# Kernel tuning notes

Measured on AMD Instinct MI355X. Metric: run time of the kernel, lower is better.

Reference implementation:

```python
import jax, jax.numpy as jnp
import numpy as np


def _banded_diag_mean(a, b, r):
    """For each (batch i, row j) return mean of (a[i] @ b[i].T)[j, j-r:j+r+1],
    computed without materializing the LxL matrix. Windows are clipped to
    [max(0,j-r), min(L, j+r+1)].  a, b: [B, L, D]."""
    B, L, _ = a.shape
    sums = jnp.zeros((B, L), a.dtype)
    counts = jnp.zeros((L,), a.dtype)
    for d in range(-r, r + 1):  # small fixed set of 2r+1 diagonals
        if d >= 0:
            dots = jnp.einsum('bld,bld->bl', a[:, :L - d], b[:, d:])
            sums = sums.at[:, :L - d].add(dots)
            counts = counts.at[:L - d].add(1.0)
        else:
            dots = jnp.einsum('bld,bld->bl', a[:, -d:], b[:, :L + d])
            sums = sums.at[:, -d:].add(dots)
            counts = counts.at[-d:].add(1.0)
    return sums / counts


def setup_inputs() -> dict:
    key = jax.random.key(0)
    k1, k2, k3 = jax.random.split(key, 3)
    B, L, D_in, D_feat = 8, 1024, 512, 256
    return {
        'feature1': jax.random.normal(k1, (B, L, D_in), jnp.float32),
        'feature2': jax.random.normal(k2, (B, L, D_in), jnp.float32),
        'W': jax.random.normal(k3, (D_in, D_feat), jnp.float32) / np.sqrt(D_in),
        'b': jnp.zeros((D_feat,), jnp.float32),
        'positive_range_self': 4,
        'positive_range_tgt': 4,
    }


def reference(feature1, feature2, W, b, positive_range_self, positive_range_tgt):
    # MLPLayer projection (shared eval_func for both inputs): linear + relu
    emb_1 = jax.nn.relu(feature1 @ W + b)  # [B, L, Df]
    emb_2 = jax.nn.relu(feature2 @ W + b)  # [B, L, Df]
    B, L, Df = emb_1.shape
    N = B * L

    positive = jnp.einsum('bld,bld->bl', emb_1, emb_2)  # [B, L]
    if positive_range_self > 0:
        positive = positive + _banded_diag_mean(emb_1, emb_1, positive_range_self)
        positive = positive + _banded_diag_mean(emb_2, emb_2, positive_range_self)
    if positive_range_tgt > 0:
        positive = positive + _banded_diag_mean(emb_1, emb_2, positive_range_tgt)
    positive = positive.reshape(N)

    e1 = emb_1.reshape(N, Df)
    e2 = emb_2.reshape(N, Df)
    sim_matrix = e1 @ e2.T  # [N, N]
    negative = jax.nn.logsumexp(sim_matrix, axis=-1) - jnp.log(jnp.asarray(N, sim_matrix.dtype))

    nce_loss = jnp.mean(-positive + negative)
    return nce_loss
```

## Files before the change

kernel.cpp:

```cpp
#include <hip/hip_runtime.h>
#include <hip/hip_bf16.h>
#include <math.h>

#define DIN 512
#define DF 256
#define LSEQ 1024
#define NTOT 8192

typedef __attribute__((ext_vector_type(8))) short short8;
typedef __attribute__((ext_vector_type(4))) short short4v;
typedef __attribute__((ext_vector_type(4))) float f32x4;

__device__ __forceinline__ short f2bf(float x) {
  union { float f; unsigned u; } un; un.f = x;
  unsigned r = un.u + 0x7fffu + ((un.u >> 16) & 1u);
  return (short)(r >> 16);
}
__device__ __forceinline__ float bf2f(short s) {
  union { unsigned u; float f; } un; un.u = ((unsigned)(unsigned short)s) << 16;
  return un.f;
}

typedef __attribute__((address_space(1))) const unsigned char AS1c;
typedef __attribute__((address_space(3))) unsigned char AS3;
__device__ __forceinline__ void gload16(const void* g, void* l) {
  __builtin_amdgcn_global_load_lds((AS1c*)g, (AS3*)l, 16, 0, 0);
}

__global__ __launch_bounds__(256) void prep_w_kernel(const float* __restrict__ W,
                                                     short* __restrict__ Wt) {
  int idx = blockIdx.x * 256 + threadIdx.x;
  int c = idx >> 9;
  int k = idx & (DIN - 1);
  Wt[idx] = f2bf(W[(size_t)k * DF + c]);
}

#define PBM 64
#define PBK 32
#define PPAD 40

__global__ __launch_bounds__(256) void proj_kernel(const float* __restrict__ f1,
                                                   const float* __restrict__ f2,
                                                   const short* __restrict__ Wt,
                                                   const float* __restrict__ bias,
                                                   short* __restrict__ emb1,
                                                   short* __restrict__ emb2) {
  const float* feat = blockIdx.y ? f2 : f1;
  short* emb = blockIdx.y ? emb2 : emb1;
  __shared__ short ldsA[PBM * PPAD];
  __shared__ short ldsB[DF * PPAD];
  const int tid = threadIdx.x;
  const int lane = tid & 63, wv = tid >> 6;
  const int wrow = (wv & 1) * 32, wcol = (wv >> 1) * 128;
  const int l15 = lane & 15, lk = (lane >> 4) * 8;
  const int rowbase = blockIdx.x * PBM;

  f32x4 acc[2][8];
#pragma unroll
  for (int mi = 0; mi < 2; ++mi)
#pragma unroll
    for (int nf = 0; nf < 8; ++nf) acc[mi][nf] = f32x4{0.f, 0.f, 0.f, 0.f};

  for (int kb = 0; kb < DIN; kb += PBK) {
    __syncthreads();
#pragma unroll
    for (int i = 0; i < 2; ++i) {
      int flat = tid * 2 + i;
      int r = flat >> 3, kq = (flat & 7) * 4;
      f32x4 v = *(const f32x4*)(feat + (size_t)(rowbase + r) * DIN + kb + kq);
      short4v h;
      h[0] = f2bf(v[0]); h[1] = f2bf(v[1]); h[2] = f2bf(v[2]); h[3] = f2bf(v[3]);
      *(short4v*)(ldsA + r * PPAD + kq) = h;
    }
#pragma unroll
    for (int i = 0; i < 4; ++i) {
      int flat = tid * 4 + i;
      int c = flat >> 2, kq = (flat & 3) * 8;
      short8 v = *(const short8*)(Wt + (size_t)c * DIN + kb + kq);
      *(short8*)(ldsB + c * PPAD + kq) = v;
    }
    __syncthreads();
    short8 af[2], bf[8];
#pragma unroll
    for (int mi = 0; mi < 2; ++mi)
      af[mi] = *(const short8*)(ldsA + (wrow + mi * 16 + l15) * PPAD + lk);
#pragma unroll
    for (int nf = 0; nf < 8; ++nf)
      bf[nf] = *(const short8*)(ldsB + (wcol + nf * 16 + l15) * PPAD + lk);
#pragma unroll
    for (int mi = 0; mi < 2; ++mi)
#pragma unroll
      for (int nf = 0; nf < 8; ++nf)
        acc[mi][nf] = __builtin_amdgcn_mfma_f32_16x16x32_bf16(af[mi], bf[nf], acc[mi][nf], 0, 0, 0);
  }
  const int r4 = (lane >> 4) * 4;
#pragma unroll
  for (int mi = 0; mi < 2; ++mi) {
    int row0 = rowbase + wrow + mi * 16 + r4;
#pragma unroll
    for (int nf = 0; nf < 8; ++nf) {
      int col = wcol + nf * 16 + l15;
      float bb = bias[col];
#pragma unroll
      for (int r = 0; r < 4; ++r) {
        float v = acc[mi][nf][r] + bb;
        v = v > 0.f ? v : 0.f;
        emb[(size_t)(row0 + r) * DF + col] = f2bf(v);
      }
    }
  }
}

__global__ __launch_bounds__(64) void positive_kernel(const short* __restrict__ emb1,
                                                      const short* __restrict__ emb2,
                                                      const int* __restrict__ prs,
                                                      const int* __restrict__ prt,
                                                      float* __restrict__ pos) {
  const int row = blockIdx.x;
  const int b = row >> 10, j = row & (LSEQ - 1);
  const int lane = threadIdx.x;
  const int rs = prs[0], rt = prt[0];
  float a1[4], a2[4];
  {
    short4v v1 = *(const short4v*)(emb1 + (size_t)row * DF + lane * 4);
    short4v v2 = *(const short4v*)(emb2 + (size_t)row * DF + lane * 4);
#pragma unroll
    for (int i = 0; i < 4; ++i) { a1[i] = bf2f(v1[i]); a2[i] = bf2f(v2[i]); }
  }
  float dot12 = 0.f, p11 = 0.f, p22 = 0.f, p12 = 0.f;
#pragma unroll
  for (int i = 0; i < 4; ++i) dot12 += a1[i] * a2[i];
  int rmax = rs > rt ? rs : rt;
  for (int d = -rmax; d <= rmax; ++d) {
    int k = j + d;
    if (k < 0 || k >= LSEQ) continue;
    size_t koff = (size_t)(b * LSEQ + k) * DF + lane * 4;
    short4v w1 = *(const short4v*)(emb1 + koff);
    short4v w2 = *(const short4v*)(emb2 + koff);
    float d11 = 0.f, d22 = 0.f, d12 = 0.f;
#pragma unroll
    for (int i = 0; i < 4; ++i) {
      float e1k = bf2f(w1[i]), e2k = bf2f(w2[i]);
      d11 += a1[i] * e1k;
      d22 += a2[i] * e2k;
      d12 += a1[i] * e2k;
    }
    if (d >= -rs && d <= rs) { p11 += d11; p22 += d22; }
    if (d >= -rt && d <= rt) { p12 += d12; }
  }
#pragma unroll
  for (int m = 1; m < 64; m <<= 1) {
    dot12 += __shfl_xor(dot12, m);
    p11 += __shfl_xor(p11, m);
    p22 += __shfl_xor(p22, m);
    p12 += __shfl_xor(p12, m);
  }
  if (lane == 0) {
    float res = dot12;
    if (rs > 0) {
      int lo = j - rs < 0 ? 0 : j - rs;
      int hi = j + rs > LSEQ - 1 ? LSEQ - 1 : j + rs;
      res += (p11 + p22) / (float)(hi - lo + 1);
    }
    if (rt > 0) {
      int lo = j - rt < 0 ? 0 : j - rt;
      int hi = j + rt > LSEQ - 1 ? LSEQ - 1 : j + rt;
      res += p12 / (float)(hi - lo + 1);
    }
    pos[row] = res;
  }
}

#define NBM 256
#define NBN 64
#define NCHUNK 16
#define CHW (NTOT / NCHUNK)
#define NT (CHW / NBN)

__global__ __launch_bounds__(256, 2) void negative_kernel(const short* __restrict__ e1,
                                                          const short* __restrict__ e2,
                                                          float* __restrict__ mpart,
                                                          float* __restrict__ spart) {
  __shared__ short ldsB[2][NBN * DF];
  const int tid = threadIdx.x;
  const int lane = tid & 63, wv = tid >> 6;
  const int l15 = lane & 15, lk16 = lane >> 4;
  const int rowbase = blockIdx.x * NBM + wv * 64;
  const int chunk = blockIdx.y;
  const short* colbase = e2 + (size_t)(chunk * CHW) * DF;

  short8 a[4][8];
#pragma unroll
  for (int mi = 0; mi < 4; ++mi)
#pragma unroll
    for (int ks = 0; ks < 8; ++ks)
      a[mi][ks] = *(const short8*)(e1 + (size_t)(rowbase + mi * 16 + l15) * DF + ks * 32 + lk16 * 8);

  float mrun[16], srun[16];
#pragma unroll
  for (int i = 0; i < 16; ++i) { mrun[i] = -1e30f; srun[i] = 0.f; }

#pragma unroll
  for (int i = 0; i < 8; ++i) {
    int L = i * 256 + tid;
    int c = L >> 5, s = L & 31;
    int kblk = s ^ (c & 31);
    gload16(colbase + (size_t)c * DF + kblk * 8, (short*)ldsB[0] + (i * 256 + wv * 64) * 8);
  }
  __syncthreads();

  for (int t = 0; t < NT; ++t) {
    short* buf = (short*)ldsB[t & 1];
    if (t + 1 < NT) {
      const short* nb = colbase + (size_t)(t + 1) * NBN * DF;
      short* dbuf = (short*)ldsB[(t + 1) & 1];
#pragma unroll
      for (int i = 0; i < 8; ++i) {
        int L = i * 256 + tid;
        int c = L >> 5, s = L & 31;
        int kblk = s ^ (c & 31);
        gload16(nb + (size_t)c * DF + kblk * 8, dbuf + (i * 256 + wv * 64) * 8);
      }
    }
    f32x4 acc[4][4];
#pragma unroll
    for (int mi = 0; mi < 4; ++mi)
#pragma unroll
      for (int nf = 0; nf < 4; ++nf) acc[mi][nf] = f32x4{0.f, 0.f, 0.f, 0.f};
#pragma unroll
    for (int ks = 0; ks < 8; ++ks) {
      short8 bfr[4];
#pragma unroll
      for (int nf = 0; nf < 4; ++nf) {
        int c = nf * 16 + l15;
        int kblk = ks * 4 + lk16;
        int s = kblk ^ (c & 31);
        bfr[nf] = *(const short8*)(buf + (c * 32 + s) * 8);
      }
#pragma unroll
      for (int mi = 0; mi < 4; ++mi)
#pragma unroll
        for (int nf = 0; nf < 4; ++nf)
          acc[mi][nf] = __builtin_amdgcn_mfma_f32_16x16x32_bf16(a[mi][ks], bfr[nf], acc[mi][nf], 0, 0, 0);
    }
#pragma unroll
    for (int mi = 0; mi < 4; ++mi)
#pragma unroll
      for (int r = 0; r < 4; ++r) {
        int s8 = mi * 4 + r;
        float v0 = acc[mi][0][r], v1 = acc[mi][1][r], v2 = acc[mi][2][r], v3 = acc[mi][3][r];
        float mx = fmaxf(fmaxf(v0, v1), fmaxf(v2, v3));
        float mo = mrun[s8];
        if (mx > mo + 8.f) {
          srun[s8] *= __expf(mo - mx);
          mo = mx;
          mrun[s8] = mx;
        }
        srun[s8] += __expf(v0 - mo) + __expf(v1 - mo) + __expf(v2 - mo) + __expf(v3 - mo);
      }
    __syncthreads();
  }
#pragma unroll
  for (int mi = 0; mi < 4; ++mi)
#pragma unroll
    for (int r = 0; r < 4; ++r) {
      int s8 = mi * 4 + r;
      float m = mrun[s8], s = srun[s8];
#pragma unroll
      for (int msk = 1; msk < 16; msk <<= 1) {
        float mo = __shfl_xor(m, msk);
        float so = __shfl_xor(s, msk);
        float mn = fmaxf(m, mo);
        s = s * __expf(m - mn) + so * __expf(mo - mn);
        m = mn;
      }
      if (l15 == 0) {
        int row = rowbase + mi * 16 + lk16 * 4 + r;
        mpart[chunk * NTOT + row] = m;
        spart[chunk * NTOT + row] = s;
      }
    }
}

__global__ __launch_bounds__(256) void finalize1_kernel(const float* __restrict__ pos,
                                                        const float* __restrict__ mpart,
                                                        const float* __restrict__ spart,
                                                        float* __restrict__ partial) {
  __shared__ float red[4];
  int row = blockIdx.x * 256 + threadIdx.x;
  float m = -1e30f;
#pragma unroll
  for (int c = 0; c < NCHUNK; ++c) m = fmaxf(m, mpart[c * NTOT + row]);
  float s = 0.f;
#pragma unroll
  for (int c = 0; c < NCHUNK; ++c) s += spart[c * NTOT + row] * __expf(mpart[c * NTOT + row] - m);
  float v = m + logf(s) - pos[row];
#pragma unroll
  for (int msk = 1; msk < 64; msk <<= 1) v += __shfl_xor(v, msk);
  if ((threadIdx.x & 63) == 0) red[threadIdx.x >> 6] = v;
  __syncthreads();
  if (threadIdx.x == 0) partial[blockIdx.x] = red[0] + red[1] + red[2] + red[3];
}

__global__ __launch_bounds__(64) void finalize2_kernel(const float* __restrict__ partial,
                                                       float* __restrict__ out) {
  int lane = threadIdx.x;
  float v = lane < 32 ? partial[lane] : 0.f;
#pragma unroll
  for (int msk = 1; msk < 64; msk <<= 1) v += __shfl_xor(v, msk);
  if (lane == 0) out[0] = v / (float)NTOT - logf((float)NTOT);
}

extern "C" void kernel_launch(void* const* d_in, const int* in_sizes, int n_in,
                              void* d_out, int out_size, void* d_ws, size_t ws_size,
                              hipStream_t stream) {
  const float* f1 = (const float*)d_in[0];
  const float* f2 = (const float*)d_in[1];
  const float* W = (const float*)d_in[2];
  const float* bias = (const float*)d_in[3];
  const int* prs = (const int*)d_in[4];
  const int* prt = (const int*)d_in[5];
  float* out = (float*)d_out;

  char* ws = (char*)d_ws;
  short* Wt = (short*)(ws);
  short* emb1 = (short*)(ws + 262144);
  short* emb2 = (short*)(ws + 262144 + 4194304);
  float* pos = (float*)(ws + 8650752);
  float* mpart = (float*)(ws + 8683520);
  float* spart = (float*)(ws + 9207808);
  float* partial = (float*)(ws + 9732096);

  prep_w_kernel<<<(DF * DIN) / 256, 256, 0, stream>>>(W, Wt);
  proj_kernel<<<dim3(NTOT / PBM, 2), 256, 0, stream>>>(f1, f2, Wt, bias, emb1, emb2);
  positive_kernel<<<NTOT, 64, 0, stream>>>(emb1, emb2, prs, prt, pos);
  negative_kernel<<<dim3(NTOT / NBM, NCHUNK), 256, 0, stream>>>(emb1, emb2, mpart, spart);
  finalize1_kernel<<<32, 256, 0, stream>>>(pos, mpart, spart, partial);
  finalize2_kernel<<<1, 64, 0, stream>>>(partial, out);
}
```

Baseline: 112.4 us.

## Restructure negative kernel pipeline with explicit waitcnt, prefetch depth two, split softmax

The negative (logsumexp) kernel now issues the first two B-tile stages up front, overlapping them with the register loads of the A operand. Each iteration waits with explicit vmcnt counters and raw s_barrier instead of __syncthreads, then prefetches tile t+2 after compute. The column tile is processed in two halves, with setprio raised around the MFMA section and the online-softmax update done per half, so exp work can interleave with matrix math. The projection kernel doubles its K tile to 64 with two MFMA sub-steps per LDS fill, halving the number of barrier rounds. The hand-written vmcnt counts rely on an exact count of outstanding loads, so a compiler reordering of loads could make them wrong.

New measurement: 107.1 us. 4.8% less time.

```diff
diff --git a/kernel.cpp b/kernel.cpp
--- a/kernel.cpp
+++ b/kernel.cpp
@@ -26,6 +26,7 @@
 __device__ __forceinline__ void gload16(const void* g, void* l) {
   __builtin_amdgcn_global_load_lds((AS1c*)g, (AS3*)l, 16, 0, 0);
 }
+#define CFENCE() asm volatile("" ::: "memory")
 
 __global__ __launch_bounds__(256) void prep_w_kernel(const float* __restrict__ W,
                                                      short* __restrict__ Wt) {
@@ -36,8 +37,8 @@
 }
 
 #define PBM 64
-#define PBK 32
-#define PPAD 40
+#define PBK 64
+#define PROW 72
 
 __global__ __launch_bounds__(256) void proj_kernel(const float* __restrict__ f1,
                                                    const float* __restrict__ f2,
@@ -47,8 +48,8 @@
                                                    short* __restrict__ emb2) {
   const float* feat = blockIdx.y ? f2 : f1;
   short* emb = blockIdx.y ? emb2 : emb1;
-  __shared__ short ldsA[PBM * PPAD];
-  __shared__ short ldsB[DF * PPAD];
+  __shared__ short ldsA[PBM * PROW];
+  __shared__ short ldsB[DF * PROW];
   const int tid = threadIdx.x;
   const int lane = tid & 63, wv = tid >> 6;
   const int wrow = (wv & 1) * 32, wcol = (wv >> 1) * 128;
@@ -64,34 +65,36 @@
   for (int kb = 0; kb < DIN; kb += PBK) {
     __syncthreads();
 #pragma unroll
-    for (int i = 0; i < 2; ++i) {
-      int flat = tid * 2 + i;
-      int r = flat >> 3, kq = (flat & 7) * 4;
+    for (int i = 0; i < 4; ++i) {
+      int flat = tid * 4 + i;
+      int r = flat >> 4, kq = (flat & 15) * 4;
       f32x4 v = *(const f32x4*)(feat + (size_t)(rowbase + r) * DIN + kb + kq);
       short4v h;
       h[0] = f2bf(v[0]); h[1] = f2bf(v[1]); h[2] = f2bf(v[2]); h[3] = f2bf(v[3]);
-      *(short4v*)(ldsA + r * PPAD + kq) = h;
-    }
-#pragma unroll
-    for (int i = 0; i < 4; ++i) {
-      int flat = tid * 4 + i;
-      int c = flat >> 2, kq = (flat & 3) * 8;
+      *(short4v*)(ldsA + r * PROW + kq) = h;
+    }
+#pragma unroll
+    for (int i = 0; i < 8; ++i) {
+      int c = tid, kq = i * 8;
       short8 v = *(const short8*)(Wt + (size_t)c * DIN + kb + kq);
-      *(short8*)(ldsB + c * PPAD + kq) = v;
+      *(short8*)(ldsB + c * PROW + kq) = v;
     }
     __syncthreads();
-    short8 af[2], bf[8];
-#pragma unroll
-    for (int mi = 0; mi < 2; ++mi)
-      af[mi] = *(const short8*)(ldsA + (wrow + mi * 16 + l15) * PPAD + lk);
-#pragma unroll
-    for (int nf = 0; nf < 8; ++nf)
-      bf[nf] = *(const short8*)(ldsB + (wcol + nf * 16 + l15) * PPAD + lk);
-#pragma unroll
-    for (int mi = 0; mi < 2; ++mi)
+#pragma unroll
+    for (int kk = 0; kk < 2; ++kk) {
+      short8 af[2], bf[8];
+#pragma unroll
+      for (int mi = 0; mi < 2; ++mi)
+        af[mi] = *(const short8*)(ldsA + (wrow + mi * 16 + l15) * PROW + kk * 32 + lk);
 #pragma unroll
       for (int nf = 0; nf < 8; ++nf)
-        acc[mi][nf] = __builtin_amdgcn_mfma_f32_16x16x32_bf16(af[mi], bf[nf], acc[mi][nf], 0, 0, 0);
+        bf[nf] = *(const short8*)(ldsB + (wcol + nf * 16 + l15) * PROW + kk * 32 + lk);
+#pragma unroll
+      for (int mi = 0; mi < 2; ++mi)
+#pragma unroll
+        for (int nf = 0; nf < 8; ++nf)
+          acc[mi][nf] = __builtin_amdgcn_mfma_f32_16x16x32_bf16(af[mi], bf[nf], acc[mi][nf], 0, 0, 0);
+    }
   }
   const int r4 = (lane >> 4) * 4;
 #pragma unroll
@@ -186,80 +189,87 @@
   const int lane = tid & 63, wv = tid >> 6;
   const int l15 = lane & 15, lk16 = lane >> 4;
   const int rowbase = blockIdx.x * NBM + wv * 64;
-  const int chunk = blockIdx.y;
-  const short* colbase = e2 + (size_t)(chunk * CHW) * DF;
-
+  const short* colbase = e2 + (size_t)(blockIdx.y * CHW) * DF;
+
+  auto stage = [&](int tt) {
+    const short* nb = colbase + (size_t)tt * NBN * DF;
+    short* db = (short*)ldsB[tt & 1];
+#pragma unroll
+    for (int i = 0; i < 8; ++i) {
+      int L = i * 256 + tid;
+      int c = L >> 5, s = L & 31;
+      int kb = s ^ (c & 31);
+      gload16(nb + (size_t)c * DF + kb * 8, db + (i * 256 + wv * 64) * 8);
+    }
+  };
+
+  stage(0);
+  CFENCE();
   short8 a[4][8];
 #pragma unroll
   for (int mi = 0; mi < 4; ++mi)
 #pragma unroll
     for (int ks = 0; ks < 8; ++ks)
       a[mi][ks] = *(const short8*)(e1 + (size_t)(rowbase + mi * 16 + l15) * DF + ks * 32 + lk16 * 8);
+  CFENCE();
+  stage(1);
+  CFENCE();
 
   float mrun[16], srun[16];
 #pragma unroll
   for (int i = 0; i < 16; ++i) { mrun[i] = -1e30f; srun[i] = 0.f; }
 
-#pragma unroll
-  for (int i = 0; i < 8; ++i) {
-    int L = i * 256 + tid;
-    int c = L >> 5, s = L & 31;
-    int kblk = s ^ (c & 31);
-    gload16(colbase + (size_t)c * DF + kblk * 8, (short*)ldsB[0] + (i * 256 + wv * 64) * 8);
-  }
-  __syncthreads();
-
   for (int t = 0; t < NT; ++t) {
-    short* buf = (short*)ldsB[t & 1];
-    if (t + 1 < NT) {
-      const short* nb = colbase + (size_t)(t + 1) * NBN * DF;
-      short* dbuf = (short*)ldsB[(t + 1) & 1];
-#pragma unroll
-      for (int i = 0; i < 8; ++i) {
-        int L = i * 256 + tid;
-        int c = L >> 5, s = L & 31;
-        int kblk = s ^ (c & 31);
-        gload16(nb + (size_t)c * DF + kblk * 8, dbuf + (i * 256 + wv * 64) * 8);
+    if (t < NT - 1) asm volatile("s_waitcnt vmcnt(8)" ::: "memory");
+    else            asm volatile("s_waitcnt vmcnt(0)" ::: "memory");
+    __builtin_amdgcn_sched_barrier(0);
+    __builtin_amdgcn_s_barrier();
+    const short* buf = (const short*)ldsB[t & 1];
+
+    f32x4 acc[4][4];
+#pragma unroll
+    for (int mi = 0; mi < 4; ++mi)
+#pragma unroll
+      for (int nf = 0; nf < 4; ++nf) acc[mi][nf] = f32x4{0.f, 0.f, 0.f, 0.f};
+
+#pragma unroll
+    for (int nfp = 0; nfp < 2; ++nfp) {
+      __builtin_amdgcn_s_setprio(1);
+#pragma unroll
+      for (int ks = 0; ks < 8; ++ks) {
+        int kblk = ks * 4 + lk16;
+        int c0 = (2 * nfp) * 16 + l15;
+        int c1 = (2 * nfp + 1) * 16 + l15;
+        short8 b0 = *(const short8*)(buf + (c0 * 32 + (kblk ^ (c0 & 31))) * 8);
+        short8 b1 = *(const short8*)(buf + (c1 * 32 + (kblk ^ (c1 & 31))) * 8);
+#pragma unroll
+        for (int mi = 0; mi < 4; ++mi) {
+          acc[mi][2 * nfp] = __builtin_amdgcn_mfma_f32_16x16x32_bf16(a[mi][ks], b0, acc[mi][2 * nfp], 0, 0, 0);
+          acc[mi][2 * nfp + 1] = __builtin_amdgcn_mfma_f32_16x16x32_bf16(a[mi][ks], b1, acc[mi][2 * nfp + 1], 0, 0, 0);
+        }
       }
-    }
-    f32x4 acc[4][4];
-#pragma unroll
-    for (int mi = 0; mi < 4; ++mi)
-#pragma unroll
-      for (int nf = 0; nf < 4; ++nf) acc[mi][nf] = f32x4{0.f, 0.f, 0.f, 0.f};
-#pragma unroll
-    for (int ks = 0; ks < 8; ++ks) {
-      short8 bfr[4];
-#pragma unroll
-      for (int nf = 0; nf < 4; ++nf) {
-        int c = nf * 16 + l15;
-        int kblk = ks * 4 + lk16;
-        int s = kblk ^ (c & 31);
-        bfr[nf] = *(const short8*)(buf + (c * 32 + s) * 8);
-      }
+      __builtin_amdgcn_s_setprio(0);
 #pragma unroll
       for (int mi = 0; mi < 4; ++mi)
 #pragma unroll
-        for (int nf = 0; nf < 4; ++nf)
-          acc[mi][nf] = __builtin_amdgcn_mfma_f32_16x16x32_bf16(a[mi][ks], bfr[nf], acc[mi][nf], 0, 0, 0);
-    }
-#pragma unroll
-    for (int mi = 0; mi < 4; ++mi)
-#pragma unroll
-      for (int r = 0; r < 4; ++r) {
-        int s8 = mi * 4 + r;
-        float v0 = acc[mi][0][r], v1 = acc[mi][1][r], v2 = acc[mi][2][r], v3 = acc[mi][3][r];
-        float mx = fmaxf(fmaxf(v0, v1), fmaxf(v2, v3));
-        float mo = mrun[s8];
-        if (mx > mo + 8.f) {
-          srun[s8] *= __expf(mo - mx);
-          mo = mx;
-          mrun[s8] = mx;
+        for (int r = 0; r < 4; ++r) {
+          int s8 = mi * 4 + r;
+          float v0 = acc[mi][2 * nfp][r], v1 = acc[mi][2 * nfp + 1][r];
+          float mx = fmaxf(v0, v1);
+          float mo = mrun[s8];
+          if (mx > mo + 8.f) {
+            srun[s8] *= __expf(mo - mx);
+            mo = mx;
+            mrun[s8] = mx;
+          }
+          srun[s8] += __expf(v0 - mo) + __expf(v1 - mo);
         }
-        srun[s8] += __expf(v0 - mo) + __expf(v1 - mo) + __expf(v2 - mo) + __expf(v3 - mo);
-      }
-    __syncthreads();
-  }
+    }
+    __builtin_amdgcn_s_barrier();
+    CFENCE();
+    if (t + 2 < NT) stage(t + 2);
+  }
+
 #pragma unroll
   for (int mi = 0; mi < 4; ++mi)
 #pragma unroll
@@ -276,8 +286,8 @@
       }
       if (l15 == 0) {
         int row = rowbase + mi * 16 + lk16 * 4 + r;
-        mpart[chunk * NTOT + row] = m;
-        spart[chunk * NTOT + row] = s;
+        mpart[blockIdx.y * NTOT + row] = m;
+        spart[blockIdx.y * NTOT + row] = s;
       }
     }
 }
```
